# Performance work log

Measured on AMD Instinct MI355X. Metric: run time of the kernel, lower is better.

The kernel has to match this reference:

```python
import jax, jax.numpy as jnp
import numpy as np

EPS = 1e-5

def mean_variance_norm(x):
    # x: [b,c,h,w]; torch .var(dim=2) on flattened spatial is UNBIASED (n-1)
    b, c, h, w = x.shape
    n = h * w
    mean = jnp.mean(x, axis=(2, 3), keepdims=True)
    var = jnp.sum((x - mean) ** 2, axis=(2, 3), keepdims=True) / (n - 1) + EPS
    return (x - mean) / jnp.sqrt(var)

def conv1x1(x, W, b):
    # 1x1 conv == channel-mixing matmul. W: [out_c, in_c], b: [out_c]
    return jnp.einsum('oc,bchw->bohw', W, x) + b[None, :, None, None]

def setup_inputs() -> dict:
    key = jax.random.key(0)
    ks = jax.random.split(key, 10)
    C = 512
    shp = (4, C, 64, 64)
    std = 1.0 / np.sqrt(C)
    return {
        'content': jax.random.normal(ks[0], shp, jnp.float32),
        'style': jax.random.normal(ks[1], shp, jnp.float32),
        'Wf': jax.random.normal(ks[2], (C, C), jnp.float32) * std,
        'bf': jax.random.normal(ks[3], (C,), jnp.float32) * 0.01,
        'Wg': jax.random.normal(ks[4], (C, C), jnp.float32) * std,
        'bg': jax.random.normal(ks[5], (C,), jnp.float32) * 0.01,
        'Wh': jax.random.normal(ks[6], (C, C), jnp.float32) * std,
        'bh': jax.random.normal(ks[7], (C,), jnp.float32) * 0.01,
        'Wo': jax.random.normal(ks[8], (C, C), jnp.float32) * std,
        'bo': jax.random.normal(ks[9], (C,), jnp.float32) * 0.01,
    }

def reference(content, style, Wf, bf, Wg, bg, Wh, bh, Wo, bo):
    b, c, h, w = content.shape
    hw = h * w
    F = conv1x1(mean_variance_norm(content), Wf, bf).reshape(b, c, hw)  # queries
    G = conv1x1(mean_variance_norm(style), Wg, bg).reshape(b, c, hw)    # keys
    H = conv1x1(style, Wh, bh).reshape(b, c, hw)                        # values
    # S[b,n,m] = sum_c F[b,c,n] * G[b,c,m]  (unscaled attention scores)
    S = jnp.einsum('bcn,bcm->bnm', F, G)
    S = jax.nn.softmax(S, axis=-1)
    # O[b,c,n] = sum_m H[b,c,m] * S[b,n,m]
    O = jnp.einsum('bcm,bnm->bcn', H, S).reshape(b, c, h, w)
    O = conv1x1(O, Wo, bo)
    return O + content
```

## Files before the change

### kernel.cpp

```cpp
#include <hip/hip_runtime.h>

#define C 512
#define HW 4096
#define EPSV 1e-5f

typedef _Float16 fp16x8 __attribute__((ext_vector_type(8)));
typedef _Float16 fp16x4 __attribute__((ext_vector_type(4)));
typedef float f32x4 __attribute__((ext_vector_type(4)));

#define OFF_MC    (0)
#define OFF_RC    (8192)
#define OFF_MS    (16384)
#define OFF_RS    (24576)
#define OFF_BETAF (32768)
#define OFF_V     (40960)
#define OFF_BZ    (49152)
#define OFF_T     (65536)
#define OFF_SP    (131072)
#define OFF_A     (OFF_SP + 2097152)
#define OFF_WZ    (OFF_A + 1048576)
#define OFF_XCT   (OFF_WZ + 1048576)
#define OFF_XST   (OFF_XCT + 16777216)
#define OFF_KT    (OFF_XST + 16777216)
#define OFF_HM    (OFF_KT + 16777216)
#define OFF_ML    (OFF_HM + 16777216)
#define OFF_S     (OFF_ML + 8388608)

#define FT_IDX(n, c) ((((size_t)((n) >> 4) * 16 + ((c) >> 5)) * 512) + \
                      ((((c) >> 3) & 3) * 128) + (((n) & 15) * 8) + ((c) & 7))

#define SFT_IDX(n, m) ((((size_t)((n) >> 4) * 128 + ((m) >> 5)) * 512) + \
                       ((((m) >> 3) & 3) * 128) + (((n) & 15) * 8) + ((m) & 7))


__global__ void transpose_stats_kernel(const float* __restrict__ xc, const float* __restrict__ xs,
                                       char* __restrict__ ws)
{
    int bx = blockIdx.x;
    int tensor = bx >> 11, b = (bx >> 9) & 3, c0 = ((bx >> 6) & 7) * 64, n0 = (bx & 63) * 64;
    const float* src = tensor ? xs : xc;
    _Float16* dst = (_Float16*)(ws + (tensor ? OFF_XST : OFF_XCT));
    float2* part = (float2*)(ws + OFF_SP);

    __shared__ _Float16 tile[64][72];
    __shared__ float pS[64][16], pSS[64][16];

    int tid = threadIdx.x, w = tid >> 6, lane = tid & 63, cq = lane >> 4, l16 = lane & 15;
    #pragma unroll
    for (int k = 0; k < 4; k++) {
        int cr = w * 16 + k * 4 + cq;
        int nf = l16 * 4;
        float4 v = *(const float4*)(src + ((size_t)(b * C + c0 + cr)) * HW + n0 + nf);
        pS[cr][l16] = v.x + v.y + v.z + v.w;
        pSS[cr][l16] = v.x * v.x + v.y * v.y + v.z * v.z + v.w * v.w;
        tile[nf][cr] = (_Float16)v.x; tile[nf + 1][cr] = (_Float16)v.y;
        tile[nf + 2][cr] = (_Float16)v.z; tile[nf + 3][cr] = (_Float16)v.w;
    }
    __syncthreads();
    if (tid < 64) {
        float S = 0.f, SS = 0.f;
        #pragma unroll
        for (int j = 0; j < 16; j++) { S += pS[tid][j]; SS += pSS[tid][j]; }
        part[((size_t)((tensor * 4 + b) * 512 + c0 + tid)) * 64 + (n0 >> 6)] =
            make_float2(S, SS);
    }
    _Float16* dstB = dst + (size_t)b * HW * C;
    #pragma unroll
    for (int i = 0; i < 2; i++) {
        int g = tid + i * 256, row = g >> 3, c8 = (g & 7) * 8;
        int n = n0 + row, c = c0 + c8;
        *(fp16x8*)&dstB[FT_IDX(n, c)] = *(const fp16x8*)&tile[row][c8];
    }
}

__global__ void finalize_stats_kernel(char* __restrict__ ws)
{
    int ch = blockIdx.x * 256 + threadIdx.x;
    const float2* part = (const float2*)(ws + OFF_SP) + (size_t)ch * 64;
    float S = 0.f, SS = 0.f;
    for (int k = 0; k < 64; k++) { float2 v = part[k]; S += v.x; SS += v.y; }
    int tensor = ch >> 11, rem = ch & 2047;
    float m = S / (float)HW;
    float var = (SS - S * m) / (float)(HW - 1) + EPSV;
    ((float*)(ws + (tensor ? OFF_MS : OFF_MC)))[rem] = m;
    ((float*)(ws + (tensor ? OFF_RS : OFF_RC)))[rem] = rsqrtf(var);
}

__global__ void precompute_kernel(const float* __restrict__ Wf, const float* __restrict__ Wg,
                                  const float* __restrict__ Wo, const float* __restrict__ Wh,
                                  const float* __restrict__ bf, const float* __restrict__ bh,
                                  char* __restrict__ ws)
{
    float* A = (float*)(ws + OFF_A);
    _Float16* Wz16 = (_Float16*)(ws + OFF_WZ);
    float* betaf = (float*)(ws + OFF_BETAF);
    float* bz = (float*)(ws + OFF_BZ);
    const float* mc = (const float*)(ws + OFF_MC);
    const float* rc = (const float*)(ws + OFF_RC);
    int bx = blockIdx.x, t = threadIdx.x;
    if (bx < 512) {
        bool isA = bx < 256;
        int r0 = (isA ? bx : bx - 256) * 2;
        float a00 = 0.f, a01 = 0.f, a10 = 0.f, a11 = 0.f;
        for (int k = 0; k < C; k++) {
            float r0v, r1v, c0v, c1v;
            if (isA) {
                r0v = Wf[k * C + r0]; r1v = Wf[k * C + r0 + 1];
                c0v = Wg[k * C + t];  c1v = Wg[k * C + t + 256];
            } else {
                r0v = Wo[r0 * C + k]; r1v = Wo[(r0 + 1) * C + k];
                c0v = Wh[k * C + t];  c1v = Wh[k * C + t + 256];
            }
            a00 += r0v * c0v; a01 += r0v * c1v;
            a10 += r1v * c0v; a11 += r1v * c1v;
        }
        if (isA) {
            A[r0 * C + t] = a00;       A[r0 * C + t + 256] = a01;
            A[(r0 + 1) * C + t] = a10; A[(r0 + 1) * C + t + 256] = a11;
        } else {
            Wz16[FT_IDX(r0, t)] = (_Float16)a00;
            Wz16[FT_IDX(r0, t + 256)] = (_Float16)a01;
            Wz16[FT_IDX(r0 + 1, t)] = (_Float16)a10;
            Wz16[FT_IDX(r0 + 1, t + 256)] = (_Float16)a11;
        }
    } else if (bx < 520) {
        int g = (bx - 512) * 256 + t, b = g >> 9, co = g & 511;
        float acc = 0.f;
        for (int i = 0; i < C; i++) acc += Wf[co * C + i] * mc[b * C + i] * rc[b * C + i];
        betaf[g] = bf[co] - acc;
    } else {
        int co = (bx - 520) * 256 + t;
        float acc = 0.f;
        for (int i = 0; i < C; i++) acc += Wo[co * C + i] * bh[i];
        bz[co] = acc;
    }
}

__global__ void scaleA_kernel(char* __restrict__ ws)
{
    const float* __restrict__ A = (const float*)(ws + OFF_A);
    const float* __restrict__ rc = (const float*)(ws + OFF_RC);
    const float* __restrict__ rs = (const float*)(ws + OFF_RS);
    _Float16* __restrict__ As = (_Float16*)(ws + OFF_SP);

    int gid = blockIdx.x * 256 + threadIdx.x;
    int b = gid >> 15, rem = gid & 32767;
    int sub = rem >> 6, low6 = rem & 63;
    int r16 = sub >> 4, cb4 = sub & 15;
    int q = low6 >> 4, l16 = low6 & 15;
    int r = r16 * 16 + l16, j0 = (cb4 * 4 + q) * 8;

    float4 a0 = *(const float4*)&A[r * C + j0];
    float4 a1 = *(const float4*)&A[r * C + j0 + 4];
    float4 s0 = *(const float4*)&rs[b * C + j0];
    float4 s1 = *(const float4*)&rs[b * C + j0 + 4];
    float rcv = rc[b * C + r];
    fp16x8 o;
    o[0] = (_Float16)(a0.x * rcv * s0.x); o[1] = (_Float16)(a0.y * rcv * s0.y);
    o[2] = (_Float16)(a0.z * rcv * s0.z); o[3] = (_Float16)(a0.w * rcv * s0.w);
    o[4] = (_Float16)(a1.x * rcv * s1.x); o[5] = (_Float16)(a1.y * rcv * s1.y);
    o[6] = (_Float16)(a1.z * rcv * s1.z); o[7] = (_Float16)(a1.w * rcv * s1.w);
    *(fp16x8*)&As[(size_t)b * 262144 + (size_t)sub * 512 + low6 * 8] = o;
}

__global__ void precompute_v_kernel(const float* __restrict__ Wg, char* __restrict__ ws)
{
    const float* betaf = (const float*)(ws + OFF_BETAF);
    const float* rs = (const float*)(ws + OFF_RS);
    float* v = (float*)(ws + OFF_V);
    int g = blockIdx.x * 32 + (threadIdx.x >> 3);
    int b = g >> 9, j = g & 511, cq = threadIdx.x & 7;
    float acc = 0.f;
    for (int co = cq * 64; co < cq * 64 + 64; co++) acc += betaf[b * C + co] * Wg[co * C + j];
    acc += __shfl_xor(acc, 1);
    acc += __shfl_xor(acc, 2);
    acc += __shfl_xor(acc, 4);
    if (cq == 0) v[g] = rs[b * C + j] * acc;
}

__global__ void __launch_bounds__(256) prep_gemm_kernel(char* __restrict__ ws)
{
    const _Float16* __restrict__ As = (const _Float16*)(ws + OFF_SP);
    const _Float16* __restrict__ Wz16 = (const _Float16*)(ws + OFF_WZ);
    const float* __restrict__ bz = (const float*)(ws + OFF_BZ);
    const _Float16* __restrict__ xsT = (const _Float16*)(ws + OFF_XST);
    _Float16* __restrict__ Kt = (_Float16*)(ws + OFF_KT);
    _Float16* __restrict__ Hp = (_Float16*)(ws + OFF_HM);

    int bx = blockIdx.x;
    int b = bx & 3, rest = bx >> 2;
    int r128 = rest >> 5, mb = rest & 31;
    int r0 = r128 * 128, m0 = mb * 128;
    int w = threadIdx.x >> 6, lane = threadIdx.x & 63, q = lane >> 4, l16 = lane & 15;
    int wr = (w & 1) * 64, wm = (w >> 1) * 64;
    bool isK = (r0 < 512);
    int rbase = (isK ? r0 : r0 - 512) + wr;

    f32x4 zz = {0.f, 0.f, 0.f, 0.f};
    f32x4 acc[4][4];
    #pragma unroll
    for (int rt = 0; rt < 4; rt++)
        #pragma unroll
        for (int mt = 0; mt < 4; mt++) acc[rt][mt] = zz;

    const _Float16* ap = (isK ? As + (size_t)b * 262144 : Wz16)
                         + (size_t)(rbase >> 4) * 8192 + q * 128 + l16 * 8;
    const _Float16* xb = xsT + (size_t)b * HW * C
                             + (size_t)((m0 + wm) >> 4) * 8192 + q * 128 + l16 * 8;

    for (int ks = 0; ks < 16; ks++) {
        fp16x8 afr[4], bfr[4];
        #pragma unroll
        for (int rt = 0; rt < 4; rt++)
            afr[rt] = *(const fp16x8*)(ap + (size_t)rt * 8192 + ks * 512);
        #pragma unroll
        for (int mt = 0; mt < 4; mt++)
            bfr[mt] = *(const fp16x8*)(xb + (size_t)(mt * 16 + ks) * 512);
        #pragma unroll
        for (int rt = 0; rt < 4; rt++)
            #pragma unroll
            for (int mt = 0; mt < 4; mt++)
                acc[rt][mt] = __builtin_amdgcn_mfma_f32_16x16x32_f16(afr[rt], bfr[mt], acc[rt][mt], 0, 0, 0);
    }

    if (isK) {
        _Float16* KtB = Kt + (size_t)b * HW * C;
        #pragma unroll
        for (int rt = 0; rt < 4; rt++)
            #pragma unroll
            for (int mt = 0; mt < 4; mt++) {
                int m = m0 + wm + mt * 16 + l16;
                int cb = r0 + wr + rt * 16 + q * 4;
                fp16x4 h;
                h[0] = (_Float16)acc[rt][mt][0]; h[1] = (_Float16)acc[rt][mt][1];
                h[2] = (_Float16)acc[rt][mt][2]; h[3] = (_Float16)acc[rt][mt][3];
                *(fp16x4*)&KtB[FT_IDX(m, cb)] = h;
            }
    } else {
        _Float16* HpB = Hp + (size_t)b * 2097152;
        #pragma unroll
        for (int rt = 0; rt < 4; rt++) {
            float bzv[4];
            #pragma unroll
            for (int reg = 0; reg < 4; reg++) bzv[reg] = bz[rbase + rt * 16 + q * 4 + reg];
            #pragma unroll
            for (int mt = 0; mt < 4; mt++) {
                int m = m0 + wm + mt * 16 + l16;
                int mbase = (m >> 3) * 128 + (m & 7);
                #pragma unroll
                for (int reg = 0; reg < 4; reg++) {
                    int co = rbase + rt * 16 + q * 4 + reg;
                    HpB[(size_t)(co >> 4) * 65536 + mbase + (co & 15) * 8] =
                        (_Float16)(acc[rt][mt][reg] + bzv[reg]);
                }
            }
        }
    }
}

__global__ void t_kernel(char* __restrict__ ws)
{
    const float* v = (const float*)(ws + OFF_V);
    const _Float16* __restrict__ xsT = (const _Float16*)(ws + OFF_XST);
    float* tG = (float*)(ws + OFF_T);
    int bx = blockIdx.x;
    int b = bx >> 6, mb = bx & 63;
    int tid = threadIdx.x, w = tid >> 6, lane = tid & 63, q = lane >> 4, l16 = lane & 15;
    int M16 = mb * 4 + w;
    const _Float16* p = xsT + (size_t)b * HW * C + (size_t)M16 * 8192 + q * 128 + l16 * 8;
    const float* vp = v + b * C + q * 8;
    float acc = 0.f;
    #pragma unroll
    for (int st = 0; st < 16; st++) {
        fp16x8 xv = *(const fp16x8*)(p + st * 512);
        float4 v0 = *(const float4*)(vp + st * 32);
        float4 v1 = *(const float4*)(vp + st * 32 + 4);
        acc += (float)xv[0] * v0.x + (float)xv[1] * v0.y + (float)xv[2] * v0.z + (float)xv[3] * v0.w
             + (float)xv[4] * v1.x + (float)xv[5] * v1.y + (float)xv[6] * v1.z + (float)xv[7] * v1.w;
    }
    acc += __shfl_xor(acc, 16);
    acc += __shfl_xor(acc, 32);
    if (q == 0) tG[b * HW + M16 * 16 + l16] = acc;
}

__global__ void __launch_bounds__(256, 4) qk_kernel(char* __restrict__ ws)
{
    const _Float16* __restrict__ xcT = (const _Float16*)(ws + OFF_XCT);
    const _Float16* __restrict__ Kt = (const _Float16*)(ws + OFF_KT);
    const float* __restrict__ tG = (const float*)(ws + OFF_T);
    float2* __restrict__ ML = (float2*)(ws + OFF_ML);
    _Float16* __restrict__ Sg = (_Float16*)(ws + OFF_S);

    int bx = blockIdx.x;
    int b = (bx >> 1) & 3, mhi = bx & 1;
    int rest = bx >> 3, mlo = rest & 15, ntile = rest >> 4;
    int m0 = (mhi * 16 + mlo) * 128, n0 = ntile * 128;
    int tid = threadIdx.x, w = tid >> 6, lane = tid & 63, q = lane >> 4, l16 = lane & 15;
    int wn = (w & 1) * 64, wm = (w >> 1) * 64;

    const _Float16* ab = xcT + (size_t)b * HW * C
                             + (size_t)((n0 + wn) >> 4) * 8192 + q * 128 + l16 * 8;
    const _Float16* bb = Kt + (size_t)b * HW * C
                            + (size_t)((m0 + wm) >> 4) * 8192 + q * 128 + l16 * 8;

    f32x4 zz = {0.f, 0.f, 0.f, 0.f};
    f32x4 acc[4][4];
    #pragma unroll
    for (int nt = 0; nt < 4; nt++)
        #pragma unroll
        for (int mt = 0; mt < 4; mt++) acc[nt][mt] = zz;

    #pragma unroll 4
    for (int ks = 0; ks < 16; ks++) {
        fp16x8 afr[4], bfr[4];
        #pragma unroll
        for (int nt = 0; nt < 4; nt++)
            afr[nt] = *(const fp16x8*)(ab + (size_t)(nt * 16 + ks) * 512);
        #pragma unroll
        for (int mt = 0; mt < 4; mt++)
            bfr[mt] = *(const fp16x8*)(bb + (size_t)(mt * 16 + ks) * 512);
        #pragma unroll
        for (int nt = 0; nt < 4; nt++)
            #pragma unroll
            for (int mt = 0; mt < 4; mt++)
                acc[nt][mt] = __builtin_amdgcn_mfma_f32_16x16x32_f16(afr[nt], bfr[mt], acc[nt][mt], 0, 0, 0);
    }

    float tv[4];
    #pragma unroll
    for (int mt = 0; mt < 4; mt++) tv[mt] = tG[b * HW + m0 + wm + mt * 16 + l16];
    #pragma unroll
    for (int nt = 0; nt < 4; nt++)
        #pragma unroll
        for (int mt = 0; mt < 4; mt++)
            #pragma unroll
            for (int reg = 0; reg < 4; reg++) acc[nt][mt][reg] += tv[mt];

    float rm[4][4], sum[4][4];
    #pragma unroll
    for (int nt = 0; nt < 4; nt++)
        #pragma unroll
        for (int reg = 0; reg < 4; reg++)
            rm[nt][reg] = fmaxf(fmaxf(acc[nt][0][reg], acc[nt][1][reg]),
                                fmaxf(acc[nt][2][reg], acc[nt][3][reg]));
    #pragma unroll
    for (int s = 1; s < 16; s <<= 1)
        #pragma unroll
        for (int nt = 0; nt < 4; nt++)
            #pragma unroll
            for (int reg = 0; reg < 4; reg++)
                rm[nt][reg] = fmaxf(rm[nt][reg], __shfl_xor(rm[nt][reg], s));
    #pragma unroll
    for (int nt = 0; nt < 4; nt++)
        #pragma unroll
        for (int reg = 0; reg < 4; reg++) sum[nt][reg] = 0.f;
    #pragma unroll
    for (int nt = 0; nt < 4; nt++)
        #pragma unroll
        for (int mt = 0; mt < 4; mt++)
            #pragma unroll
            for (int reg = 0; reg < 4; reg++) {
                float pv = __expf(acc[nt][mt][reg] - rm[nt][reg]);
                acc[nt][mt][reg] = pv;
                sum[nt][reg] += pv;
            }
    #pragma unroll
    for (int s = 1; s < 16; s <<= 1)
        #pragma unroll
        for (int nt = 0; nt < 4; nt++)
            #pragma unroll
            for (int reg = 0; reg < 4; reg++)
                sum[nt][reg] += __shfl_xor(sum[nt][reg], s);

    int tl = (m0 + wm) >> 6;
    if (l16 == 0) {
        #pragma unroll
        for (int nt = 0; nt < 4; nt++)
            #pragma unroll
            for (int reg = 0; reg < 4; reg++)
                ML[((size_t)(b * HW + n0 + wn + nt * 16 + q * 4 + reg)) * 64 + tl] =
                    make_float2(rm[nt][reg], sum[nt][reg]);
    }

    __shared__ _Float16 Pl[4][64][72];
    #pragma unroll
    for (int nt = 0; nt < 4; nt++)
        #pragma unroll
        for (int mt = 0; mt < 4; mt++)
            #pragma unroll
            for (int reg = 0; reg < 4; reg++)
                Pl[w][nt * 16 + q * 4 + reg][mt * 16 + l16] = (_Float16)acc[nt][mt][reg];
    __syncthreads();
    _Float16* SgB = Sg + (size_t)b * 16777216;
    #pragma unroll
    for (int i = 0; i < 8; i++) {
        int row = i * 8 + (lane >> 3), c8 = (lane & 7) * 8;
        int n = n0 + wn + row, m = m0 + wm + c8;
        *(fp16x8*)&SgB[SFT_IDX(n, m)] = *(const fp16x8*)&Pl[w][row][c8];
    }
}

__global__ void __launch_bounds__(256) scale_kernel(char* __restrict__ ws)
{
    const float* __restrict__ mlf0 = (const float*)(ws + OFF_ML);
    float* __restrict__ Scl = (float*)(ws + OFF_XCT);
    __shared__ float mlv[64][129];
    __shared__ float Ms[64], Li[64];

    int g0 = blockIdx.x * 64;
    int tid = threadIdx.x;
    const float* mlf = mlf0 + (size_t)g0 * 128;

    #pragma unroll
    for (int i = 0; i < 8; i++) {
        int f4 = i * 256 + tid;
        int row = f4 >> 5, c4 = (f4 & 31) * 4;
        float4 v = *(const float4*)(mlf + row * 128 + c4);
        mlv[row][c4] = v.x; mlv[row][c4 + 1] = v.y;
        mlv[row][c4 + 2] = v.z; mlv[row][c4 + 3] = v.w;
    }
    __syncthreads();
    if (tid < 64) {
        float M = -1e30f;
        #pragma unroll
        for (int k = 0; k < 64; k++) M = fmaxf(M, mlv[tid][k * 2]);
        float L = 0.f;
        #pragma unroll
        for (int k = 0; k < 64; k++) L += mlv[tid][k * 2 + 1] * __expf(mlv[tid][k * 2] - M);
        Ms[tid] = M; Li[tid] = 1.f / L;
    }
    __syncthreads();
    int b = g0 >> 12, nbase = g0 & 4095;
    float* sp = Scl + (size_t)b * 262144 + nbase;
    int row = tid & 63, tsub = tid >> 6;
    #pragma unroll
    for (int pass = 0; pass < 16; pass++) {
        int tile = pass * 4 + tsub;
        sp[(size_t)tile * 4096 + row] = __expf(mlv[row][tile * 2] - Ms[row]) * Li[row];
    }
}

__global__ void __launch_bounds__(256, 4) pv_kernel(const float* __restrict__ xc,
                                                    const float* __restrict__ bo,
                                                    float* __restrict__ out,
                                                    char* __restrict__ ws)
{
    const _Float16* __restrict__ Sft = (const _Float16*)(ws + OFF_S);
    const _Float16* __restrict__ Hp = (const _Float16*)(ws + OFF_HM);
    const float* __restrict__ Scl = (const float*)(ws + OFF_XCT);

    int bx = blockIdx.x;
    int b = bx & 3, cog = (bx >> 2) & 7, ntb = bx >> 5;
    int co0 = cog * 64;
    int tid = threadIdx.x, w = tid >> 6, lane = tid & 63, q = lane >> 4, l16 = lane & 15;
    int n0w = ntb * 128 + w * 32;

    __shared__ _Float16 Hl[2][4096];

    int ln64 = lane;
    const _Float16* hsrc = Hp + (size_t)b * 2097152
                              + (size_t)((co0 >> 4) + w) * 65536 + ln64 * 8;
    const _Float16* sb = Sft + (size_t)b * 16777216
                             + (size_t)(ntb * 8 + w * 2) * 65536 + q * 128 + l16 * 8;
    const float* sc = Scl + (size_t)b * 262144 + n0w + q * 4;

    {
        fp16x8 s0 = *(const fp16x8*)(hsrc);
        fp16x8 s1 = *(const fp16x8*)(hsrc + 512);
        *(fp16x8*)&Hl[0][w * 1024 + ln64 * 8] = s0;
        *(fp16x8*)&Hl[0][w * 1024 + 512 + ln64 * 8] = s1;
    }
    __syncthreads();

    f32x4 zz = {0.f, 0.f, 0.f, 0.f};
    f32x4 acc[2][4];
    #pragma unroll
    for (int nt = 0; nt < 2; nt++)
        #pragma unroll
        for (int ct = 0; ct < 4; ct++) acc[nt][ct] = zz;

    for (int chunk = 0; chunk < 64; chunk++) {
        int buf = chunk & 1;
        fp16x8 s0n, s1n;
        if (chunk < 63) {
            s0n = *(const fp16x8*)(hsrc + (chunk + 1) * 1024);
            s1n = *(const fp16x8*)(hsrc + (chunk + 1) * 1024 + 512);
        }

        f32x4 tmp[2][4];
        #pragma unroll
        for (int km = 0; km < 2; km++) {
            fp16x8 afr[2], bfr[4];
            #pragma unroll
            for (int nt = 0; nt < 2; nt++)
                afr[nt] = *(const fp16x8*)(sb + (size_t)nt * 65536 + (chunk * 2 + km) * 512);
            #pragma unroll
            for (int ct = 0; ct < 4; ct++)
                bfr[ct] = *(const fp16x8*)&Hl[buf][ct * 1024 + (km * 4 + q) * 128 + l16 * 8];
            #pragma unroll
            for (int nt = 0; nt < 2; nt++)
                #pragma unroll
                for (int ct = 0; ct < 4; ct++)
                    tmp[nt][ct] = __builtin_amdgcn_mfma_f32_16x16x32_f16(
                        afr[nt], bfr[ct], km == 0 ? zz : tmp[nt][ct], 0, 0, 0);
        }
        float4 sv0 = *(const float4*)(sc + chunk * 4096);
        float4 sv1 = *(const float4*)(sc + chunk * 4096 + 16);
        float sva[2][4] = {{sv0.x, sv0.y, sv0.z, sv0.w}, {sv1.x, sv1.y, sv1.z, sv1.w}};
        #pragma unroll
        for (int nt = 0; nt < 2; nt++)
            #pragma unroll
            for (int ct = 0; ct < 4; ct++)
                #pragma unroll
                for (int reg = 0; reg < 4; reg++)
                    acc[nt][ct][reg] += tmp[nt][ct][reg] * sva[nt][reg];

        if (chunk < 63) {
            *(fp16x8*)&Hl[buf ^ 1][w * 1024 + ln64 * 8] = s0n;
            *(fp16x8*)&Hl[buf ^ 1][w * 1024 + 512 + ln64 * 8] = s1n;
        }
        __syncthreads();
    }

    #pragma unroll
    for (int nt = 0; nt < 2; nt++)
        #pragma unroll
        for (int ct = 0; ct < 4; ct++) {
            int co = co0 + ct * 16 + l16;
            size_t base = ((size_t)(b * C + co)) * HW + n0w + nt * 16 + q * 4;
            float4 cv = *(const float4*)&xc[base];
            float bov = bo[co];
            float4 o;
            o.x = acc[nt][ct][0] + bov + cv.x;
            o.y = acc[nt][ct][1] + bov + cv.y;
            o.z = acc[nt][ct][2] + bov + cv.z;
            o.w = acc[nt][ct][3] + bov + cv.w;
            *(float4*)&out[base] = o;
        }
}

extern "C" void kernel_launch(void* const* d_in, const int* in_sizes, int n_in,
                              void* d_out, int out_size, void* d_ws, size_t ws_size,
                              hipStream_t stream)
{
    const float* content = (const float*)d_in[0];
    const float* style   = (const float*)d_in[1];
    const float* Wf = (const float*)d_in[2];
    const float* bf = (const float*)d_in[3];
    const float* Wg = (const float*)d_in[4];
    const float* Wh = (const float*)d_in[6];
    const float* bh = (const float*)d_in[7];
    const float* Wo = (const float*)d_in[8];
    const float* bo = (const float*)d_in[9];
    float* out = (float*)d_out;
    char* ws = (char*)d_ws;

    transpose_stats_kernel<<<4096, 256, 0, stream>>>(content, style, ws);
    finalize_stats_kernel<<<16, 256, 0, stream>>>(ws);
    precompute_kernel<<<522, 256, 0, stream>>>(Wf, Wg, Wo, Wh, bf, bh, ws);
    scaleA_kernel<<<512, 256, 0, stream>>>(ws);
    precompute_v_kernel<<<64, 256, 0, stream>>>(Wg, ws);
    prep_gemm_kernel<<<1024, 256, 0, stream>>>(ws);
    t_kernel<<<256, 256, 0, stream>>>(ws);
    qk_kernel<<<4096, 256, 0, stream>>>(ws);
    scale_kernel<<<256, 256, 0, stream>>>(ws);
    pv_kernel<<<1024, 256, 0, stream>>>(content, bo, out, ws);
}
```

Measured before the change: 463.2 us.

## Stage QK operand tiles through double-buffered LDS with register prefetch

The QK score kernel now loads A and B operand tiles cooperatively into shared memory, double-buffered, and prefetches the next k-step into registers while the current step's MFMAs run. Previously each wave read its fragments straight from global memory, so waves sharing the same rows or columns loaded that data redundantly. The LDS buffer is reused for the output staging array. The change adds a barrier every k-step and raises shared-memory use, which may lower occupancy under the 4-blocks launch bound.

```diff
diff --git a/kernel.cpp b/kernel.cpp
--- a/kernel.cpp
+++ b/kernel.cpp
@@ -298,10 +298,23 @@
     int tid = threadIdx.x, w = tid >> 6, lane = tid & 63, q = lane >> 4, l16 = lane & 15;
     int wn = (w & 1) * 64, wm = (w >> 1) * 64;
 
-    const _Float16* ab = xcT + (size_t)b * HW * C
-                             + (size_t)((n0 + wn) >> 4) * 8192 + q * 128 + l16 * 8;
-    const _Float16* bb = Kt + (size_t)b * HW * C
-                            + (size_t)((m0 + wm) >> 4) * 8192 + q * 128 + l16 * 8;
+    __shared__ char lbuf[36864];
+    _Float16* Ax0 = (_Float16*)lbuf;
+    _Float16* Bx0 = (_Float16*)(lbuf + 16384);
+
+    int st = tid >> 5, so = (tid & 31) * 16;
+    const _Float16* gA = xcT + (size_t)b * HW * C + ((size_t)(n0 >> 4) + st) * 8192 + so;
+    const _Float16* gB = Kt + (size_t)b * HW * C + ((size_t)(m0 >> 4) + st) * 8192 + so;
+
+    {
+        fp16x8 a0 = *(const fp16x8*)(gA);
+        fp16x8 a1 = *(const fp16x8*)(gA + 8);
+        fp16x8 b0 = *(const fp16x8*)(gB);
+        fp16x8 b1 = *(const fp16x8*)(gB + 8);
+        *(fp16x8*)&Ax0[tid * 16] = a0; *(fp16x8*)&Ax0[tid * 16 + 8] = a1;
+        *(fp16x8*)&Bx0[tid * 16] = b0; *(fp16x8*)&Bx0[tid * 16 + 8] = b1;
+    }
+    __syncthreads();
 
     f32x4 zz = {0.f, 0.f, 0.f, 0.f};
     f32x4 acc[4][4];
@@ -310,20 +323,41 @@
         #pragma unroll
         for (int mt = 0; mt < 4; mt++) acc[nt][mt] = zz;
 
-    #pragma unroll 4
+    int aoff = ((wn >> 4)) * 512 + q * 128 + l16 * 8;
+    int boff = ((wm >> 4)) * 512 + q * 128 + l16 * 8;
+
     for (int ks = 0; ks < 16; ks++) {
+        int buf = ks & 1;
+        _Float16* Axc = Ax0 + buf * 4096;
+        _Float16* Bxc = Bx0 + buf * 4096;
+        fp16x8 a0n, a1n, b0n, b1n;
+        if (ks < 15) {
+            a0n = *(const fp16x8*)(gA + (ks + 1) * 512);
+            a1n = *(const fp16x8*)(gA + (ks + 1) * 512 + 8);
+            b0n = *(const fp16x8*)(gB + (ks + 1) * 512);
+            b1n = *(const fp16x8*)(gB + (ks + 1) * 512 + 8);
+        }
+
         fp16x8 afr[4], bfr[4];
         #pragma unroll
         for (int nt = 0; nt < 4; nt++)
-            afr[nt] = *(const fp16x8*)(ab + (size_t)(nt * 16 + ks) * 512);
+            afr[nt] = *(const fp16x8*)&Axc[aoff + nt * 512];
         #pragma unroll
         for (int mt = 0; mt < 4; mt++)
-            bfr[mt] = *(const fp16x8*)(bb + (size_t)(mt * 16 + ks) * 512);
+            bfr[mt] = *(const fp16x8*)&Bxc[boff + mt * 512];
         #pragma unroll
         for (int nt = 0; nt < 4; nt++)
             #pragma unroll
             for (int mt = 0; mt < 4; mt++)
                 acc[nt][mt] = __builtin_amdgcn_mfma_f32_16x16x32_f16(afr[nt], bfr[mt], acc[nt][mt], 0, 0, 0);
+
+        if (ks < 15) {
+            _Float16* Axn = Ax0 + (buf ^ 1) * 4096;
+            _Float16* Bxn = Bx0 + (buf ^ 1) * 4096;
+            *(fp16x8*)&Axn[tid * 16] = a0n; *(fp16x8*)&Axn[tid * 16 + 8] = a1n;
+            *(fp16x8*)&Bxn[tid * 16] = b0n; *(fp16x8*)&Bxn[tid * 16 + 8] = b1n;
+        }
+        __syncthreads();
     }
 
     float tv[4];
@@ -382,7 +416,7 @@
                     make_float2(rm[nt][reg], sum[nt][reg]);
     }
 
-    __shared__ _Float16 Pl[4][64][72];
+    _Float16 (*Pl)[64][72] = (_Float16(*)[64][72])lbuf;
     #pragma unroll
     for (int nt = 0; nt < 4; nt++)
         #pragma unroll
```

Measured after the change: 459.5 us. About the same (-0.8%).
